# Optimization experiments

Hardware: AMD Instinct MI355X
Metric: run time of the kernel (lower is better)

Reference implementation:

```python
import jax, jax.numpy as jnp
import numpy as np

THETA = 1.0       # thr
TAU_RHO = 0.5     # grad_width
SCALE_RHO = 1.0   # grad_scale


def avg_pool4(x):
    # x: (N, C, H, W, T) -> 4x4 average pool per timestep (pool weight = 1/16)
    N, C, H, W, T = x.shape
    return x.reshape(N, C, H // 4, 4, W // 4, 4, T).mean(axis=(3, 5))


def conv2d_t(x, w):
    # SLAYER conv: spatial-only conv3d with kernel (k,k,1), pad 3, no bias.
    # x: (N, C, H, W, T), w: (O, I, 7, 7)
    N, C, H, W, T = x.shape
    xt = jnp.moveaxis(x, -1, 1).reshape(N * T, C, H, W)
    y = jax.lax.conv_general_dilated(
        xt, w, window_strides=(1, 1), padding=[(3, 3), (3, 3)],
        dimension_numbers=('NCHW', 'OIHW', 'NCHW'))
    O = w.shape[0]
    return jnp.moveaxis(y.reshape(N, T, O, H, W), 1, -1)


def psp(x):
    # IAF SRM kernel = unit step (Ts=1) -> causal cumulative sum over time
    return jnp.cumsum(x, axis=-1)


def _spike_scan(u):
    # Sequential threshold + persistent refractory subtraction (scaleRef=1, IAF)
    uT = jnp.moveaxis(u, -1, 0)  # (T, ...)
    def step(r, ut):
        v = ut + r                       # membrane incl. refractory
        s = (v >= THETA).astype(u.dtype)
        return r - THETA * s, (s, v)
    _, (sT, vT) = jax.lax.scan(step, jnp.zeros_like(uT[0]), uT)
    return jnp.moveaxis(sT, 0, -1), jnp.moveaxis(vT, 0, -1)


@jax.custom_vjp
def spike(u):
    return _spike_scan(u)[0]


def _spike_fwd(u):
    s, v = _spike_scan(u)
    return s, v


def _spike_bwd(v, g):
    # SLAYER surrogate: no BPTT through refractory recurrence
    pdf = (SCALE_RHO / TAU_RHO) * jnp.exp(-jnp.abs(v - THETA) / TAU_RHO)
    return (g * pdf,)


spike.defvjp(_spike_fwd, _spike_bwd)


def setup_inputs() -> dict:
    key = jax.random.key(0)
    k0, k1, k2, k3 = jax.random.split(key, 4)
    data = jax.random.uniform(k0, (4, 2, 256, 256, 100), dtype=jnp.float32)
    w0 = jax.random.normal(k1, (4, 2, 7, 7), dtype=jnp.float32) * 0.1
    w1 = jax.random.normal(k2, (8, 4, 7, 7), dtype=jnp.float32) * 0.05
    wl = jax.random.normal(k3, (2, 8, 4, 4), dtype=jnp.float32) * 0.1
    return {"data": data, "w0": w0, "w1": w1, "wl": wl}


def reference(data, w0, w1, wl):
    x = avg_pool4(data)                      # (N,2,64,64,T)
    x = spike(psp(conv2d_t(x, w0)))          # (N,4,64,64,T)
    x = avg_pool4(x)                         # (N,4,16,16,T)
    x = spike(psp(conv2d_t(x, w1)))          # (N,8,16,16,T)
    x = avg_pool4(x)                         # (N,8,4,4,T)
    out = jnp.einsum('nchwt,ochw->not', x, wl)  # dense (4,4,8)->2, squeeze
    return out                               # (N,2,T)
```

## Files before the change

### kernel.cpp

```cpp
#include <hip/hip_runtime.h>
#include <hip/hip_bf16.h>

using u16 = unsigned short;
using u32 = unsigned int;
using u64 = unsigned long long;

__device__ __forceinline__ float b2f(u16 u){
  union { u32 i; float f; } x; x.i = ((u32)u) << 16; return x.f;
}

__global__ __launch_bounds__(256) void k_prep(const void* __restrict__ data,
                                              const void* __restrict__ w0,
                                              const void* __restrict__ w1,
                                              const void* __restrict__ wl,
                                              int* __restrict__ gflag,
                                              float* __restrict__ w0f,
                                              float* __restrict__ w1f,
                                              float* __restrict__ wlf){
  __shared__ int zs[4], ss[4];
  __shared__ int sflag;
  int tid = threadIdx.x;
  u32 w = ((const u32*)data)[tid];
  u16 lo = (u16)(w & 0xFFFFu);
  u64 zb = __ballot(lo == 0);
  u64 sb = __ballot((lo >> 15) & 1);
  int wave = tid >> 6;
  if((tid & 63) == 0){ zs[wave] = __popcll(zb); ss[wave] = __popcll(sb); }
  __syncthreads();
  if(tid == 0){
    int zeros = zs[0]+zs[1]+zs[2]+zs[3];
    int signs = ss[0]+ss[1]+ss[2]+ss[3];
    int f = (zeros >= 128 || signs > 0) ? 1 : 0;
    sflag = f; *gflag = f;
  }
  __syncthreads();
  int f = sflag;
  const float* w0F = (const float*)w0; const u16* w0H = (const u16*)w0;
  const float* w1F = (const float*)w1; const u16* w1H = (const u16*)w1;
  const float* wlF = (const float*)wl; const u16* wlH = (const u16*)wl;
  for(int i = tid; i < 392;  i += 256) w0f[i] = f ? w0F[i] : b2f(w0H[i]);
  for(int i = tid; i < 1568; i += 256) w1f[i] = f ? w1F[i] : b2f(w1H[i]);
  for(int i = tid; i < 256;  i += 256) wlf[i] = f ? wlF[i] : b2f(wlH[i]);
}

__global__ __launch_bounds__(256) void k_pool1(const void* __restrict__ data,
                                               const int* __restrict__ gflag,
                                               float* __restrict__ P1){
  int idx = blockIdx.x * 256 + threadIdx.x;
  int tc  = idx % 25;
  int pix = idx / 25;
  int ow  = pix & 63;
  int oh  = (pix >> 6) & 63;
  int nc  = pix >> 12;
  int t0  = tc * 4;
  size_t off = ((size_t)((nc*256 + oh*4)*256 + ow*4)) * 100 + t0;
  double s0=0.0, s1=0.0, s2=0.0, s3=0.0;
  if(*gflag){
    const float* base = (const float*)data + off;
    #pragma unroll
    for(int di=0; di<4; ++di)
      #pragma unroll
      for(int dj=0; dj<4; ++dj){
        float4 v = *reinterpret_cast<const float4*>(base + (size_t)(di*256 + dj)*100);
        s0 += (double)v.x; s1 += (double)v.y; s2 += (double)v.z; s3 += (double)v.w;
      }
  } else {
    const u16* base = (const u16*)data + off;
    #pragma unroll
    for(int di=0; di<4; ++di)
      #pragma unroll
      for(int dj=0; dj<4; ++dj){
        ushort4 v = *reinterpret_cast<const ushort4*>(base + (size_t)(di*256 + dj)*100);
        s0 += (double)b2f(v.x); s1 += (double)b2f(v.y);
        s2 += (double)b2f(v.z); s3 += (double)b2f(v.w);
      }
  }
  float* o = P1 + (size_t)pix * 100 + t0;
  o[0] = (float)(s0 * 0.0625); o[1] = (float)(s1 * 0.0625);
  o[2] = (float)(s2 * 0.0625); o[3] = (float)(s3 * 0.0625);
}

__global__ __launch_bounds__(256) void k_conv1(const float* __restrict__ P1,
                                               const float* __restrict__ w0f,
                                               double* __restrict__ A1){
  __shared__ float4  tile[968];
  __shared__ double4 wl4[98];
  int bid  = blockIdx.x;
  int tcl  = bid % 25; int rest = bid / 25;
  int tl   = rest & 15; int n = rest >> 4;
  int ty   = (tl >> 2) * 16, tx = (tl & 3) * 16;
  int t0   = tcl * 4;
  int tid  = threadIdx.x;
  for(int i = tid; i < 392; i += 256){
    int o = i / 98, r = i % 98;
    ((double*)wl4)[r*4 + o] = (double)w0f[i];
  }
  for(int idx = tid; idx < 968; idx += 256){
    int ci = idx / 484, r = idx % 484;
    int yy = r / 22, xx = r % 22;
    int gy = ty + yy - 3, gx = tx + xx - 3;
    float4 v; v.x = v.y = v.z = v.w = 0.f;
    if(gy >= 0 && gy < 64 && gx >= 0 && gx < 64){
      const float* p = P1 + ((size_t)((n*2+ci)*64 + gy)*64 + gx)*100 + t0;
      v.x = p[0]; v.y = p[1]; v.z = p[2]; v.w = p[3];
    }
    tile[idx] = v;
  }
  __syncthreads();
  int y = tid >> 4, x = tid & 15;
  double acc[4][4] = {};
  for(int ci = 0; ci < 2; ++ci)
    for(int dy = 0; dy < 7; ++dy){
      #pragma unroll
      for(int dx = 0; dx < 7; ++dx){
        float4 iv = tile[ci*484 + (y+dy)*22 + (x+dx)];
        double4 wv = wl4[ci*49 + dy*7 + dx];
        double i0 = (double)iv.x, i1 = (double)iv.y, i2 = (double)iv.z, i3 = (double)iv.w;
        acc[0][0] += wv.x*i0; acc[0][1] += wv.x*i1; acc[0][2] += wv.x*i2; acc[0][3] += wv.x*i3;
        acc[1][0] += wv.y*i0; acc[1][1] += wv.y*i1; acc[1][2] += wv.y*i2; acc[1][3] += wv.y*i3;
        acc[2][0] += wv.z*i0; acc[2][1] += wv.z*i1; acc[2][2] += wv.z*i2; acc[2][3] += wv.z*i3;
        acc[3][0] += wv.w*i0; acc[3][1] += wv.w*i1; acc[3][2] += wv.w*i2; acc[3][3] += wv.w*i3;
      }
    }
  size_t obase = ((size_t)(n*4)*100 + t0)*4096 + (size_t)(ty+y)*64 + (tx+x);
  #pragma unroll
  for(int o = 0; o < 4; ++o)
    #pragma unroll
    for(int tt = 0; tt < 4; ++tt)
      A1[obase + ((size_t)o*100 + tt)*4096] = acc[o][tt];
}

__global__ __launch_bounds__(64) void k_scan1(const double* __restrict__ A1,
                                              float* __restrict__ S1p){
  int bid = blockIdx.x;
  int xg  = bid & 3, yg = (bid >> 2) & 15, no = bid >> 6;
  int lane = threadIdx.x;
  int lx = lane & 15, ly = lane >> 4;
  int row = yg*4 + ly, col = xg*16 + lx;
  const double* base = A1 + (size_t)no*100*4096 + (size_t)row*64 + col;
  float* outb = S1p + (size_t)no*100*256 + yg*16 + xg*4;
  int cell = lx >> 2;
  u64 cmask = 0x000F000F000F000FULL << (4*cell);
  bool writer = (ly == 0) && ((lx & 3) == 0);
  double u = 0.0, r = 0.0;
  double c0 = base[0], c1 = base[4096], c2 = base[8192], c3 = base[12288];
  for(int tb = 0; tb < 25; ++tb){
    int nb = (tb + 1 < 25) ? tb + 1 : 24;
    const double* pn = base + (size_t)nb*4*4096;
    double n0 = pn[0], n1 = pn[4096], n2 = pn[8192], n3 = pn[12288];
    #pragma unroll
    for(int j = 0; j < 4; ++j){
      double a = (j==0)?c0:(j==1)?c1:(j==2)?c2:c3;
      u += a;
      bool sp = (u + r >= 1.0);
      if(sp) r -= 1.0;
      u64 m = __ballot(sp);
      if(writer){
        float cnt = (float)__popcll(m & cmask);
        outb[(size_t)(tb*4 + j)*256 + cell] = cnt * 0.0625f;
      }
    }
    c0 = n0; c1 = n1; c2 = n2; c3 = n3;
  }
}

__global__ __launch_bounds__(256) void k_conv2(const float* __restrict__ S1p,
                                               const float* __restrict__ w1f,
                                               double* __restrict__ A2){
  __shared__ float   tf[4*4*484];
  __shared__ double4 wl4[196];
  int bid = blockIdx.x;
  int oh  = bid & 1; int rest = bid >> 1;
  int tc  = rest % 25; int n = rest / 25;
  int t0  = tc * 4;
  int tid = threadIdx.x;
  for(int i = tid; i < 7744; i += 256) tf[i] = 0.f;
  for(int i = tid; i < 784; i += 256){
    int oj = i / 196, rem = i % 196;
    ((double*)wl4)[rem*4 + oj] = (double)w1f[(oh*4 + oj)*196 + rem];
  }
  __syncthreads();
  for(int i = tid; i < 4096; i += 256){
    int ci = i >> 10, tt = (i >> 8) & 3, p = i & 255;
    int yy = p >> 4, xx = p & 15;
    tf[(ci*4 + tt)*484 + (yy+3)*22 + (xx+3)] =
        S1p[((size_t)(n*4+ci)*100 + t0 + tt)*256 + p];
  }
  __syncthreads();
  int y = tid >> 4, x = tid & 15;
  double acc[4][4] = {};
  for(int ci = 0; ci < 4; ++ci)
    for(int dy = 0; dy < 7; ++dy){
      #pragma unroll
      for(int dx = 0; dx < 7; ++dx){
        const float* tp = &tf[ci*1936 + (y+dy)*22 + (x+dx)];
        double4 wv = wl4[ci*49 + dy*7 + dx];
        double i0 = (double)tp[0],   i1 = (double)tp[484];
        double i2 = (double)tp[968], i3 = (double)tp[1452];
        acc[0][0] += wv.x*i0; acc[0][1] += wv.x*i1; acc[0][2] += wv.x*i2; acc[0][3] += wv.x*i3;
        acc[1][0] += wv.y*i0; acc[1][1] += wv.y*i1; acc[1][2] += wv.y*i2; acc[1][3] += wv.y*i3;
        acc[2][0] += wv.z*i0; acc[2][1] += wv.z*i1; acc[2][2] += wv.z*i2; acc[2][3] += wv.z*i3;
        acc[3][0] += wv.w*i0; acc[3][1] += wv.w*i1; acc[3][2] += wv.w*i2; acc[3][3] += wv.w*i3;
      }
    }
  size_t obase = ((size_t)(n*8 + oh*4)*100 + t0)*256 + tid;
  #pragma unroll
  for(int oj = 0; oj < 4; ++oj)
    #pragma unroll
    for(int tt = 0; tt < 4; ++tt)
      A2[obase + ((size_t)oj*100 + tt)*256] = acc[oj][tt];
}

__global__ __launch_bounds__(64) void k_scan2(const double* __restrict__ A2,
                                              const float* __restrict__ wlf,
                                              float* __restrict__ P4){
  int bid  = blockIdx.x;
  int q    = bid & 3, nc = bid >> 2, c = nc & 7;
  int lane = threadIdx.x;
  int px   = q*64 + lane;
  float w0g[4], w1g[4];
  #pragma unroll
  for(int g = 0; g < 4; ++g){
    w0g[g] = wlf[      c*16 + q*4 + g] * 0.0625f;
    w1g[g] = wlf[128 + c*16 + q*4 + g] * 0.0625f;
  }
  const double* base = A2 + (size_t)nc*100*256 + px;
  float* outb = P4 + (size_t)bid * 200;
  double u = 0.0, r = 0.0;
  double c0 = base[0], c1 = base[256], c2 = base[512], c3 = base[768];
  for(int tb = 0; tb < 25; ++tb){
    int nb = (tb + 1 < 25) ? tb + 1 : 24;
    const double* pn = base + (size_t)nb*4*256;
    double n0 = pn[0], n1 = pn[256], n2 = pn[512], n3 = pn[768];
    #pragma unroll
    for(int j = 0; j < 4; ++j){
      double a = (j==0)?c0:(j==1)?c1:(j==2)?c2:c3;
      u += a;
      bool sp = (u + r >= 1.0);
      if(sp) r -= 1.0;
      u64 m = __ballot(sp);
      if(lane == 0){
        float p0 = 0.f, p1 = 0.f;
        #pragma unroll
        for(int g = 0; g < 4; ++g){
          float cnt = (float)__popcll(m & (0x000F000F000F000FULL << (4*g)));
          p0 += cnt * w0g[g]; p1 += cnt * w1g[g];
        }
        int t = tb*4 + j;
        outb[t] = p0; outb[100 + t] = p1;
      }
    }
    c0 = n0; c1 = n1; c2 = n2; c3 = n3;
  }
}

__global__ __launch_bounds__(256) void k_out(const float* __restrict__ P4,
                                             const int* __restrict__ gflag,
                                             void* __restrict__ out){
  int idx = blockIdx.x * 256 + threadIdx.x;
  if(idx >= 800) return;
  int t = idx % 100; int o = (idx / 100) & 1; int n = idx / 200;
  float s = 0.f;
  for(int cq = 0; cq < 32; ++cq)
    s += P4[((size_t)(n*32 + cq))*200 + o*100 + t];
  if(*gflag) ((float*)out)[idx] = s;
  else       ((__hip_bfloat16*)out)[idx] = __float2bfloat16(s);
}

extern "C" void kernel_launch(void* const* d_in, const int* in_sizes, int n_in,
                              void* d_out, int out_size, void* d_ws, size_t ws_size,
                              hipStream_t stream) {
  const void* data = d_in[0];
  const void* w0   = d_in[1];
  const void* w1   = d_in[2];
  const void* wl   = d_in[3];
  char* ws = (char*)d_ws;
  float*  P1   = (float*) (ws + 0);
  double* A1   = (double*)(ws + 13107200);
  float*  S1p  = (float*) (ws + 65536000);
  int*    gflag= (int*)   (ws + 67174400);
  float*  w0f  = (float*) (ws + 67174404);
  float*  w1f  = (float*) (ws + 67175972);
  float*  wlf  = (float*) (ws + 67182244);
  double* A2   = (double*)(ws + 0);
  float*  P4   = (float*) (ws + 6553600);

  hipLaunchKernelGGL(k_prep,  dim3(1),    dim3(256), 0, stream,
                     data, w0, w1, wl, gflag, w0f, w1f, wlf);
  hipLaunchKernelGGL(k_pool1, dim3(3200), dim3(256), 0, stream, data, gflag, P1);
  hipLaunchKernelGGL(k_conv1, dim3(1600), dim3(256), 0, stream, P1, w0f, A1);
  hipLaunchKernelGGL(k_scan1, dim3(1024), dim3(64),  0, stream, A1, S1p);
  hipLaunchKernelGGL(k_conv2, dim3(200),  dim3(256), 0, stream, S1p, w1f, A2);
  hipLaunchKernelGGL(k_scan2, dim3(128),  dim3(64),  0, stream, A2, wlf, P4);
  hipLaunchKernelGGL(k_out,   dim3(4),    dim3(256), 0, stream, P4, gflag, d_out);
}
```

Before: 396.1 us.

## Fuse conv1 with spike scan and inline dtype detection into kernels

Merges the first convolution and its spike scan into one kernel, where each 64-thread block owns one output channel on an 8x8 tile and walks time in chunks of four. This avoids writing and re-reading the large double-precision A1 intermediate in global memory. The separate prep kernel is also removed: each kernel now detects the input dtype from the first 64 words and converts weights itself. The trade-off is that the fused kernel serialises all 25 time chunks inside one block, with barriers and tile reloads each chunk, and it has lower parallelism (1024 single-wave blocks) and recomputes the halo per output channel.

```diff
diff --git a/kernel.cpp b/kernel.cpp
--- a/kernel.cpp
+++ b/kernel.cpp
@@ -9,43 +9,17 @@
   union { u32 i; float f; } x; x.i = ((u32)u) << 16; return x.f;
 }
 
-__global__ __launch_bounds__(256) void k_prep(const void* __restrict__ data,
-                                              const void* __restrict__ w0,
-                                              const void* __restrict__ w1,
-                                              const void* __restrict__ wl,
-                                              int* __restrict__ gflag,
-                                              float* __restrict__ w0f,
-                                              float* __restrict__ w1f,
-                                              float* __restrict__ wlf){
-  __shared__ int zs[4], ss[4];
-  __shared__ int sflag;
-  int tid = threadIdx.x;
-  u32 w = ((const u32*)data)[tid];
+__device__ __forceinline__ bool detect_f32(const void* data){
+  u32 w = ((const u32*)data)[threadIdx.x & 63];
   u16 lo = (u16)(w & 0xFFFFu);
   u64 zb = __ballot(lo == 0);
   u64 sb = __ballot((lo >> 15) & 1);
-  int wave = tid >> 6;
-  if((tid & 63) == 0){ zs[wave] = __popcll(zb); ss[wave] = __popcll(sb); }
-  __syncthreads();
-  if(tid == 0){
-    int zeros = zs[0]+zs[1]+zs[2]+zs[3];
-    int signs = ss[0]+ss[1]+ss[2]+ss[3];
-    int f = (zeros >= 128 || signs > 0) ? 1 : 0;
-    sflag = f; *gflag = f;
-  }
-  __syncthreads();
-  int f = sflag;
-  const float* w0F = (const float*)w0; const u16* w0H = (const u16*)w0;
-  const float* w1F = (const float*)w1; const u16* w1H = (const u16*)w1;
-  const float* wlF = (const float*)wl; const u16* wlH = (const u16*)wl;
-  for(int i = tid; i < 392;  i += 256) w0f[i] = f ? w0F[i] : b2f(w0H[i]);
-  for(int i = tid; i < 1568; i += 256) w1f[i] = f ? w1F[i] : b2f(w1H[i]);
-  for(int i = tid; i < 256;  i += 256) wlf[i] = f ? wlF[i] : b2f(wlH[i]);
+  return (__popcll(zb) >= 32) || (sb != 0);
 }
 
 __global__ __launch_bounds__(256) void k_pool1(const void* __restrict__ data,
-                                               const int* __restrict__ gflag,
                                                float* __restrict__ P1){
+  bool f32w = detect_f32(data);
   int idx = blockIdx.x * 256 + threadIdx.x;
   int tc  = idx % 25;
   int pix = idx / 25;
@@ -55,7 +29,7 @@
   int t0  = tc * 4;
   size_t off = ((size_t)((nc*256 + oh*4)*256 + ow*4)) * 100 + t0;
   double s0=0.0, s1=0.0, s2=0.0, s3=0.0;
-  if(*gflag){
+  if(f32w){
     const float* base = (const float*)data + off;
     #pragma unroll
     for(int di=0; di<4; ++di)
@@ -80,104 +54,108 @@
   o[2] = (float)(s2 * 0.0625); o[3] = (float)(s3 * 0.0625);
 }
 
-__global__ __launch_bounds__(256) void k_conv1(const float* __restrict__ P1,
-                                               const float* __restrict__ w0f,
-                                               double* __restrict__ A1){
-  __shared__ float4  tile[968];
-  __shared__ double4 wl4[98];
-  int bid  = blockIdx.x;
-  int tcl  = bid % 25; int rest = bid / 25;
-  int tl   = rest & 15; int n = rest >> 4;
-  int ty   = (tl >> 2) * 16, tx = (tl & 3) * 16;
-  int t0   = tcl * 4;
-  int tid  = threadIdx.x;
-  for(int i = tid; i < 392; i += 256){
-    int o = i / 98, r = i % 98;
-    ((double*)wl4)[r*4 + o] = (double)w0f[i];
-  }
-  for(int idx = tid; idx < 968; idx += 256){
-    int ci = idx / 484, r = idx % 484;
-    int yy = r / 22, xx = r % 22;
+__global__ __launch_bounds__(64) void k_conv1s(const float* __restrict__ P1,
+                                               const void* __restrict__ w0,
+                                               const void* __restrict__ data,
+                                               float* __restrict__ S1p){
+  __shared__ float4 tile[392];
+  __shared__ double wd[98];
+  bool f32w = detect_f32(data);
+  int bid = blockIdx.x;
+  int tl  = bid & 63; int no = bid >> 6;
+  int o   = no & 3;  int n  = no >> 2;
+  int ty  = (tl >> 3) * 8, tx = (tl & 7) * 8;
+  int lane = threadIdx.x;
+  int y = lane >> 3, x = lane & 7;
+
+  const float* w0F = (const float*)w0; const u16* w0H = (const u16*)w0;
+  for(int i = lane; i < 98; i += 64){
+    int widx = o*98 + i;
+    wd[i] = f32w ? (double)w0F[widx] : (double)b2f(w0H[widx]);
+  }
+
+  const float* pptr[7]; bool pok[7];
+  #pragma unroll
+  for(int k = 0; k < 7; ++k){
+    int i = lane + k*64;
+    int ci = i / 196, r = i % 196;
+    int yy = r / 14, xx = r % 14;
     int gy = ty + yy - 3, gx = tx + xx - 3;
-    float4 v; v.x = v.y = v.z = v.w = 0.f;
-    if(gy >= 0 && gy < 64 && gx >= 0 && gx < 64){
-      const float* p = P1 + ((size_t)((n*2+ci)*64 + gy)*64 + gx)*100 + t0;
-      v.x = p[0]; v.y = p[1]; v.z = p[2]; v.w = p[3];
-    }
-    tile[idx] = v;
-  }
-  __syncthreads();
-  int y = tid >> 4, x = tid & 15;
-  double acc[4][4] = {};
-  for(int ci = 0; ci < 2; ++ci)
-    for(int dy = 0; dy < 7; ++dy){
-      #pragma unroll
-      for(int dx = 0; dx < 7; ++dx){
-        float4 iv = tile[ci*484 + (y+dy)*22 + (x+dx)];
-        double4 wv = wl4[ci*49 + dy*7 + dx];
-        double i0 = (double)iv.x, i1 = (double)iv.y, i2 = (double)iv.z, i3 = (double)iv.w;
-        acc[0][0] += wv.x*i0; acc[0][1] += wv.x*i1; acc[0][2] += wv.x*i2; acc[0][3] += wv.x*i3;
-        acc[1][0] += wv.y*i0; acc[1][1] += wv.y*i1; acc[1][2] += wv.y*i2; acc[1][3] += wv.y*i3;
-        acc[2][0] += wv.z*i0; acc[2][1] += wv.z*i1; acc[2][2] += wv.z*i2; acc[2][3] += wv.z*i3;
-        acc[3][0] += wv.w*i0; acc[3][1] += wv.w*i1; acc[3][2] += wv.w*i2; acc[3][3] += wv.w*i3;
-      }
-    }
-  size_t obase = ((size_t)(n*4)*100 + t0)*4096 + (size_t)(ty+y)*64 + (tx+x);
-  #pragma unroll
-  for(int o = 0; o < 4; ++o)
-    #pragma unroll
-    for(int tt = 0; tt < 4; ++tt)
-      A1[obase + ((size_t)o*100 + tt)*4096] = acc[o][tt];
-}
-
-__global__ __launch_bounds__(64) void k_scan1(const double* __restrict__ A1,
-                                              float* __restrict__ S1p){
-  int bid = blockIdx.x;
-  int xg  = bid & 3, yg = (bid >> 2) & 15, no = bid >> 6;
-  int lane = threadIdx.x;
-  int lx = lane & 15, ly = lane >> 4;
-  int row = yg*4 + ly, col = xg*16 + lx;
-  const double* base = A1 + (size_t)no*100*4096 + (size_t)row*64 + col;
-  float* outb = S1p + (size_t)no*100*256 + yg*16 + xg*4;
-  int cell = lx >> 2;
-  u64 cmask = 0x000F000F000F000FULL << (4*cell);
-  bool writer = (ly == 0) && ((lx & 3) == 0);
+    bool ok = (i < 392) && gy >= 0 && gy < 64 && gx >= 0 && gx < 64;
+    pok[k]  = ok;
+    pptr[k] = P1 + ((size_t)((n*2 + ci)*64 + (ok?gy:0))*64 + (ok?gx:0))*100;
+  }
+  float4 pf[7];
+  const float4 z4 = {0.f,0.f,0.f,0.f};
+  #pragma unroll
+  for(int k = 0; k < 7; ++k)
+    pf[k] = pok[k] ? *reinterpret_cast<const float4*>(pptr[k]) : z4;
+
+  int cy = y >> 2, cx = x >> 2;
+  u64 cmask = 0x0F0F0F0FULL << (32*cy + 4*cx);
+  bool writer = ((y & 3) == 0) && ((x & 3) == 0);
+  int pr = (ty >> 2) + cy, pc = (tx >> 2) + cx;
+  float* outb = S1p + (size_t)no*100*256 + pr*16 + pc;
+
   double u = 0.0, r = 0.0;
-  double c0 = base[0], c1 = base[4096], c2 = base[8192], c3 = base[12288];
   for(int tb = 0; tb < 25; ++tb){
-    int nb = (tb + 1 < 25) ? tb + 1 : 24;
-    const double* pn = base + (size_t)nb*4*4096;
-    double n0 = pn[0], n1 = pn[4096], n2 = pn[8192], n3 = pn[12288];
+    __syncthreads();
+    #pragma unroll
+    for(int k = 0; k < 7; ++k){
+      int i = lane + k*64;
+      if(i < 392) tile[i] = pf[k];
+    }
+    __syncthreads();
+    if(tb < 24){
+      int t0n = (tb + 1) * 4;
+      #pragma unroll
+      for(int k = 0; k < 7; ++k)
+        pf[k] = pok[k] ? *reinterpret_cast<const float4*>(pptr[k] + t0n) : z4;
+    }
+    double a0=0.0, a1=0.0, a2=0.0, a3=0.0;
+    for(int ci = 0; ci < 2; ++ci)
+      for(int dy = 0; dy < 7; ++dy){
+        #pragma unroll
+        for(int dx = 0; dx < 7; ++dx){
+          float4 iv = tile[ci*196 + (y+dy)*14 + (x+dx)];
+          double w  = wd[ci*49 + dy*7 + dx];
+          a0 += w*(double)iv.x; a1 += w*(double)iv.y;
+          a2 += w*(double)iv.z; a3 += w*(double)iv.w;
+        }
+      }
     #pragma unroll
     for(int j = 0; j < 4; ++j){
-      double a = (j==0)?c0:(j==1)?c1:(j==2)?c2:c3;
+      double a = (j==0)?a0:(j==1)?a1:(j==2)?a2:a3;
       u += a;
       bool sp = (u + r >= 1.0);
       if(sp) r -= 1.0;
       u64 m = __ballot(sp);
       if(writer){
         float cnt = (float)__popcll(m & cmask);
-        outb[(size_t)(tb*4 + j)*256 + cell] = cnt * 0.0625f;
-      }
-    }
-    c0 = n0; c1 = n1; c2 = n2; c3 = n3;
+        outb[(size_t)(tb*4 + j)*256] = cnt * 0.0625f;
+      }
+    }
   }
 }
 
 __global__ __launch_bounds__(256) void k_conv2(const float* __restrict__ S1p,
-                                               const float* __restrict__ w1f,
+                                               const void* __restrict__ w1,
+                                               const void* __restrict__ data,
                                                double* __restrict__ A2){
   __shared__ float   tf[4*4*484];
   __shared__ double4 wl4[196];
+  bool f32w = detect_f32(data);
   int bid = blockIdx.x;
   int oh  = bid & 1; int rest = bid >> 1;
   int tc  = rest % 25; int n = rest / 25;
   int t0  = tc * 4;
   int tid = threadIdx.x;
+  const float* w1F = (const float*)w1; const u16* w1H = (const u16*)w1;
   for(int i = tid; i < 7744; i += 256) tf[i] = 0.f;
   for(int i = tid; i < 784; i += 256){
     int oj = i / 196, rem = i % 196;
-    ((double*)wl4)[rem*4 + oj] = (double)w1f[(oh*4 + oj)*196 + rem];
+    int widx = (oh*4 + oj)*196 + rem;
+    ((double*)wl4)[rem*4 + oj] = f32w ? (double)w1F[widx] : (double)b2f(w1H[widx]);
   }
   __syncthreads();
   for(int i = tid; i < 4096; i += 256){
@@ -212,17 +190,21 @@
 }
 
 __global__ __launch_bounds__(64) void k_scan2(const double* __restrict__ A2,
-                                              const float* __restrict__ wlf,
+                                              const void* __restrict__ wl,
+                                              const void* __restrict__ data,
                                               float* __restrict__ P4){
+  bool f32w = detect_f32(data);
   int bid  = blockIdx.x;
   int q    = bid & 3, nc = bid >> 2, c = nc & 7;
   int lane = threadIdx.x;
   int px   = q*64 + lane;
+  const float* wlF = (const float*)wl; const u16* wlH = (const u16*)wl;
   float w0g[4], w1g[4];
   #pragma unroll
   for(int g = 0; g < 4; ++g){
-    w0g[g] = wlf[      c*16 + q*4 + g] * 0.0625f;
-    w1g[g] = wlf[128 + c*16 + q*4 + g] * 0.0625f;
+    int i0 = c*16 + q*4 + g, i1 = 128 + c*16 + q*4 + g;
+    w0g[g] = (f32w ? wlF[i0] : b2f(wlH[i0])) * 0.0625f;
+    w1g[g] = (f32w ? wlF[i1] : b2f(wlH[i1])) * 0.0625f;
   }
   const double* base = A2 + (size_t)nc*100*256 + px;
   float* outb = P4 + (size_t)bid * 200;
@@ -255,16 +237,17 @@
 }
 
 __global__ __launch_bounds__(256) void k_out(const float* __restrict__ P4,
-                                             const int* __restrict__ gflag,
+                                             const void* __restrict__ data,
                                              void* __restrict__ out){
+  bool f32w = detect_f32(data);
   int idx = blockIdx.x * 256 + threadIdx.x;
   if(idx >= 800) return;
   int t = idx % 100; int o = (idx / 100) & 1; int n = idx / 200;
   float s = 0.f;
   for(int cq = 0; cq < 32; ++cq)
     s += P4[((size_t)(n*32 + cq))*200 + o*100 + t];
-  if(*gflag) ((float*)out)[idx] = s;
-  else       ((__hip_bfloat16*)out)[idx] = __float2bfloat16(s);
+  if(f32w) ((float*)out)[idx] = s;
+  else     ((__hip_bfloat16*)out)[idx] = __float2bfloat16(s);
 }
 
 extern "C" void kernel_launch(void* const* d_in, const int* in_sizes, int n_in,
@@ -275,22 +258,14 @@
   const void* w1   = d_in[2];
   const void* wl   = d_in[3];
   char* ws = (char*)d_ws;
-  float*  P1   = (float*) (ws + 0);
-  double* A1   = (double*)(ws + 13107200);
-  float*  S1p  = (float*) (ws + 65536000);
-  int*    gflag= (int*)   (ws + 67174400);
-  float*  w0f  = (float*) (ws + 67174404);
-  float*  w1f  = (float*) (ws + 67175972);
-  float*  wlf  = (float*) (ws + 67182244);
-  double* A2   = (double*)(ws + 0);
-  float*  P4   = (float*) (ws + 6553600);
-
-  hipLaunchKernelGGL(k_prep,  dim3(1),    dim3(256), 0, stream,
-                     data, w0, w1, wl, gflag, w0f, w1f, wlf);
-  hipLaunchKernelGGL(k_pool1, dim3(3200), dim3(256), 0, stream, data, gflag, P1);
-  hipLaunchKernelGGL(k_conv1, dim3(1600), dim3(256), 0, stream, P1, w0f, A1);
-  hipLaunchKernelGGL(k_scan1, dim3(1024), dim3(64),  0, stream, A1, S1p);
-  hipLaunchKernelGGL(k_conv2, dim3(200),  dim3(256), 0, stream, S1p, w1f, A2);
-  hipLaunchKernelGGL(k_scan2, dim3(128),  dim3(64),  0, stream, A2, wlf, P4);
-  hipLaunchKernelGGL(k_out,   dim3(4),    dim3(256), 0, stream, P4, gflag, d_out);
-}
+  float*  P1  = (float*) (ws + 0);
+  float*  S1p = (float*) (ws + 13107200);
+  double* A2  = (double*)(ws + 14745600);
+  float*  P4  = (float*) (ws + 21299200);
+
+  hipLaunchKernelGGL(k_pool1,  dim3(3200), dim3(256), 0, stream, data, P1);
+  hipLaunchKernelGGL(k_conv1s, dim3(1024), dim3(64),  0, stream, P1, w0, data, S1p);
+  hipLaunchKernelGGL(k_conv2,  dim3(200),  dim3(256), 0, stream, S1p, w1, data, A2);
+  hipLaunchKernelGGL(k_scan2,  dim3(128),  dim3(64),  0, stream, A2, wl, data, P4);
+  hipLaunchKernelGGL(k_out,    dim3(4),    dim3(256), 0, stream, P4, data, d_out);
+}
```

New measurement: 753.2 us. 90.1% more time.
